# Kernel tuning notes

Measured on AMD Instinct MI355X. Metric: run time of the kernel, lower is better.

## Reference

```python
import jax, jax.numpy as jnp
import numpy as np


def setup_inputs() -> dict:
    key = jax.random.key(0)
    ks = jax.random.split(key, 6)
    B, S, D, F, E = 4, 2048, 1024, 4096, 4
    sd = 1.0 / np.sqrt(D)
    sf = 1.0 / np.sqrt(F)
    return {
        "x": jax.random.normal(ks[0], (B, S, D), jnp.float32),
        "router_w": jax.random.normal(ks[1], (D, E), jnp.float32) * sd,
        "w1": jax.random.normal(ks[2], (E, D, F), jnp.float32) * sd,
        "b1": jnp.zeros((E, F), jnp.float32),
        "w2": jax.random.normal(ks[3], (E, F, D), jnp.float32) * sf,
        "b2": jnp.zeros((E, D), jnp.float32),
    }


def reference(x, router_w, w1, b1, w2, b2):
    # x: [B, S, D] token stream; causal MoE with top-1 routing.
    B, S, D = x.shape
    E = w1.shape[0]
    # Causal routing context: prefix mean over the sequence (causal augmenter).
    denom = jnp.arange(1, S + 1, dtype=x.dtype)[None, :, None]  # [1, S, 1]
    ctx = jnp.cumsum(x, axis=1) / denom                          # [B, S, D]
    logits = jnp.einsum("bsd,de->bse", ctx, router_w)            # [B, S, E]
    probs = jax.nn.softmax(logits, axis=-1)
    idx = jnp.argmax(probs, axis=-1)                             # top-1 expert id [B, S]
    gate = jnp.take_along_axis(probs, idx[..., None], axis=-1)   # [B, S, 1]
    onehot = jax.nn.one_hot(idx, E, dtype=x.dtype)               # [B, S, E]
    # Dispatch/combine: per-expert FFN, masked combine (loop over small fixed E).
    y = jnp.zeros_like(x)
    for e in range(E):
        h = jax.nn.gelu(jnp.einsum("bsd,df->bsf", x, w1[e]) + b1[e])
        y_e = jnp.einsum("bsf,fd->bsd", h, w2[e]) + b2[e]
        y = y + onehot[..., e:e + 1] * y_e
    return gate * y
```

## Files before the change

### kernel.cpp

```cpp
#include <hip/hip_runtime.h>
#include <math.h>

#define B_ 4
#define S_ 2048
#define D_ 1024
#define F_ 4096
#define E_ 4
#define T_ (B_*S_)
#define PCAP_ 9216
#define GCAP_ (PCAP_/16)
#define MB128_ (PCAP_/128)

typedef unsigned short ushort_t;
typedef __attribute__((ext_vector_type(8))) short short8;
typedef __attribute__((ext_vector_type(4))) float f32x4;

__device__ __forceinline__ ushort_t f2bf_rne(float f) {
    unsigned u = __float_as_uint(f);
    unsigned r = 0x7FFFu + ((u >> 16) & 1u);
    u += r;
    return (ushort_t)(u >> 16);
}

__device__ __forceinline__ void gload16(const void* g, void* l) {
    __builtin_amdgcn_global_load_lds(
        (const __attribute__((address_space(1))) unsigned int*)g,
        (__attribute__((address_space(3))) unsigned int*)l, 16, 0, 0);
}


__global__ void k_router(const float* __restrict__ x, const float* __restrict__ rw,
                         float* __restrict__ r, int* __restrict__ counts) {
    if (blockIdx.x == 0 && threadIdx.x < E_) counts[threadIdx.x] = 0;
    int wid = blockIdx.x * 4 + (threadIdx.x >> 6);
    int lane = threadIdx.x & 63;
    const float* xr = x + (size_t)wid * D_;
    float a0 = 0.f, a1 = 0.f, a2 = 0.f, a3 = 0.f;
    for (int i = lane; i < D_; i += 64) {
        float xv = xr[i];
        float4 w = reinterpret_cast<const float4*>(rw)[i];
        a0 += xv * w.x; a1 += xv * w.y; a2 += xv * w.z; a3 += xv * w.w;
    }
    for (int off = 32; off; off >>= 1) {
        a0 += __shfl_down(a0, off, 64);
        a1 += __shfl_down(a1, off, 64);
        a2 += __shfl_down(a2, off, 64);
        a3 += __shfl_down(a3, off, 64);
    }
    if (lane == 0) {
        float4 v; v.x = a0; v.y = a1; v.z = a2; v.w = a3;
        reinterpret_cast<float4*>(r)[wid] = v;
    }
}

__global__ void k_scan(float* __restrict__ r) {
    int b = blockIdx.x >> 2, e = blockIdx.x & 3;
    int lane = threadIdx.x;
    float carry = 0.f;
    for (int c = 0; c < S_ / 64; ++c) {
        int s = c * 64 + lane;
        float* p = r + ((size_t)(b * S_ + s)) * E_ + e;
        float v = *p;
        #pragma unroll
        for (int off = 1; off < 64; off <<= 1) {
            float u = __shfl_up(v, off, 64);
            if (lane >= off) v += u;
        }
        v += carry;
        *p = v;
        carry = __shfl(v, 63, 64);
    }
}

__global__ void k_route(const float* __restrict__ r, float* __restrict__ gate,
                        int* __restrict__ list, int* __restrict__ counts) {
    int t = blockIdx.x * blockDim.x + threadIdx.x;
    if (t >= T_) return;
    int s = t & (S_ - 1);
    float4 l4 = reinterpret_cast<const float4*>(r)[t];
    float inv = 1.f / (float)(s + 1);
    float l[4] = { l4.x * inv, l4.y * inv, l4.z * inv, l4.w * inv };
    int best = 0; float m = l[0];
    #pragma unroll
    for (int e = 1; e < 4; ++e) if (l[e] > m) { m = l[e]; best = e; }
    float sum = 0.f;
    #pragma unroll
    for (int e = 0; e < 4; ++e) sum += expf(l[e] - m);
    gate[t] = 1.f / sum;
    int pos = atomicAdd(&counts[best], 1);
    list[best * T_ + pos] = t;
}

__global__ void k_offs(const int* __restrict__ counts, int* __restrict__ offs,
                       int* __restrict__ pbase) {
    if (threadIdx.x == 0) {
        int a = 0, p = 0;
        pbase[0] = 0;
        for (int e = 0; e < E_; ++e) {
            offs[e] = a; a += counts[e];
            p += (counts[e] + 255) & ~255;
            pbase[e + 1] = p;
        }
    }
}

__global__ __launch_bounds__(256)
void k_gather1(const float* __restrict__ x, const int* __restrict__ list,
               const int* __restrict__ counts, const int* __restrict__ pbase,
               ushort_t* __restrict__ Xb)
{
    constexpr int KB = D_ / 32;
    const int g = blockIdx.x;
    const int r15 = threadIdx.x & 15;
    const int kq = threadIdx.x >> 4;
    const int v = g * 16 + r15;
    int e = 0;
    #pragma unroll
    for (int i = 0; i < E_; ++i) if (v >= pbase[i + 1]) e = i + 1;
    int token = -1;
    if (e < E_) {
        int local = v - pbase[e];
        if (local < counts[e]) token = list[e * T_ + local];
    }
    const float* xr = x + (size_t)(token >= 0 ? token : 0) * D_;
    #pragma unroll
    for (int c8 = 0; c8 < 8; ++c8) {
        const int k = kq * 64 + c8 * 8;
        float vv[8];
        if (token >= 0) {
            float4 u0 = *reinterpret_cast<const float4*>(xr + k);
            float4 u1 = *reinterpret_cast<const float4*>(xr + k + 4);
            vv[0]=u0.x; vv[1]=u0.y; vv[2]=u0.z; vv[3]=u0.w;
            vv[4]=u1.x; vv[5]=u1.y; vv[6]=u1.z; vv[7]=u1.w;
        } else {
            #pragma unroll
            for (int j = 0; j < 8; ++j) vv[j] = 0.f;
        }
        unsigned hw[4];
        #pragma unroll
        for (int j = 0; j < 4; ++j)
            hw[j] = (unsigned)f2bf_rne(vv[2*j]) | ((unsigned)f2bf_rne(vv[2*j+1]) << 16);
        size_t off = (((size_t)g * KB + (k >> 5)) * 64 + ((k >> 3) & 3) * 16 + r15) * 8;
        *reinterpret_cast<uint4*>(Xb + off) = make_uint4(hw[0], hw[1], hw[2], hw[3]);
    }
}

__global__ __launch_bounds__(256)
void k_convert_w1(const float* __restrict__ W, ushort_t* __restrict__ P,
                  int K, int N) {
    const int e = blockIdx.z;
    const int n0 = blockIdx.x * 128;
    const int k0 = blockIdx.y * 32;
    const int kb = blockIdx.y;
    const int NT = N >> 4, KB = K >> 5;
    __shared__ float lf[32 * 128];
    const float* We = W + (size_t)e * K * N;
    const int tid = threadIdx.x;
    #pragma unroll
    for (int i = 0; i < 4; ++i) {
        int q = i * 256 + tid;
        int k = q >> 5, c4 = q & 31;
        float4 v = *reinterpret_cast<const float4*>(We + (size_t)(k0 + k) * N + n0 + c4 * 4);
        *reinterpret_cast<float4*>(lf + k * 128 + c4 * 4) = v;
    }
    __syncthreads();
    #pragma unroll
    for (int p = 0; p < 2; ++p) {
        int q = p * 256 + tid;
        int n = q & 127, kg = q >> 7;
        unsigned hw[4];
        #pragma unroll
        for (int j = 0; j < 8; j += 2) {
            float f0 = lf[(kg * 8 + j) * 128 + n];
            float f1 = lf[(kg * 8 + j + 1) * 128 + n];
            hw[j >> 1] = (unsigned)f2bf_rne(f0) | ((unsigned)f2bf_rne(f1) << 16);
        }
        size_t off = ((((size_t)e * NT + ((n0 + n) >> 4)) * KB + kb) * 64
                      + (kg * 16 + (n & 15))) * 8;
        *reinterpret_cast<uint4*>(P + off) = make_uint4(hw[0], hw[1], hw[2], hw[3]);
    }
}

template<int MODE>
__global__ __launch_bounds__(512)
void k_gI(const ushort_t* __restrict__ A, const ushort_t* __restrict__ Bw,
          const float* __restrict__ bias, float* __restrict__ outF,
          ushort_t* __restrict__ outH,
          const int* __restrict__ list, const int* __restrict__ counts,
          const int* __restrict__ pbase, const float* __restrict__ gate)
{
    constexpr int K    = (MODE == 0) ? D_ : F_;
    constexpr int N    = (MODE == 0) ? F_ : D_;
    constexpr int KSEG = (MODE == 0) ? K : K / 2;
    constexpr int STEPS = KSEG / 32;
    constexpr int KB32 = K / 32;
    constexpr int NT   = N / 16;
    constexpr int KBH  = F_ / 32;

    const int m0g = blockIdx.x * 128;
    if (m0g >= pbase[E_]) return;
    int e = 0;
    #pragma unroll
    for (int i = 1; i <= 3; ++i) if (m0g >= pbase[i]) e = i;
    const int cnt = counts[e];
    const int m0 = m0g - pbase[e];
    if (m0 >= cnt) return;
    const int n0 = blockIdx.y * 128;
    const int kth = (MODE == 0) ? 0 : blockIdx.z;
    const int koff = kth * (KSEG / 32);

    const int tid = threadIdx.x, wid = tid >> 6, lane = tid & 63;
    const int l15 = lane & 15, lkg = lane >> 4;
    const int wr = wid >> 2, wc = wid & 3;
    const int G0 = m0g >> 4;

    __shared__ __align__(16) ushort_t lds[16 * 512];

    const ushort_t* aP = A + ((size_t)(G0 + wid) * KB32 + koff) * 512 + (size_t)lane * 8;
    const ushort_t* bP = Bw + (((size_t)e * NT + (n0 >> 4) + wid) * KB32 + koff) * 512
                            + (size_t)lane * 8;

    f32x4 acc[4][2];
    #pragma unroll
    for (int i = 0; i < 4; ++i)
        #pragma unroll
        for (int j = 0; j < 2; ++j) acc[i][j] = (f32x4){0.f, 0.f, 0.f, 0.f};

    for (int t = 0; t < STEPS; ++t) {
        __syncthreads();
        const size_t so = (size_t)t * 512;
        gload16(aP + so, &lds[wid * 512]);
        gload16(bP + so, &lds[(8 + wid) * 512]);
        __syncthreads();
        short8 av[4], bv[2];
        #pragma unroll
        for (int mi = 0; mi < 4; ++mi)
            av[mi] = *reinterpret_cast<const short8*>(
                &lds[(wr * 4 + mi) * 512 + lane * 8]);
        #pragma unroll
        for (int ni = 0; ni < 2; ++ni)
            bv[ni] = *reinterpret_cast<const short8*>(
                &lds[(8 + wc * 2 + ni) * 512 + lane * 8]);
        #pragma unroll
        for (int mi = 0; mi < 4; ++mi)
            #pragma unroll
            for (int ni = 0; ni < 2; ++ni)
                acc[mi][ni] = __builtin_amdgcn_mfma_f32_16x16x32_bf16(
                    av[mi], bv[ni], acc[mi][ni], 0, 0, 0);
    }

    const float* be = bias + (size_t)e * N;
    if (MODE == 0) {
        #pragma unroll
        for (int mi = 0; mi < 4; ++mi) {
            const int g2 = G0 + wr * 4 + mi;
            #pragma unroll
            for (int rg = 0; rg < 4; ++rg) {
                const int r15o = lkg * 4 + rg;
                #pragma unroll
                for (int ni = 0; ni < 2; ++ni) {
                    const int f = n0 + wc * 32 + ni * 16 + l15;
                    float v = acc[mi][ni][rg] + be[f];
                    float u = 1.5957691216057308f * (v + 0.044715f * v * v * v);
                    v = v / (1.f + __expf(-u));
                    size_t off = (((size_t)g2 * KBH + (f >> 5)) * 64
                                  + ((f >> 3) & 3) * 16 + r15o) * 8 + (f & 7);
                    outH[off] = f2bf_rne(v);
                }
            }
        }
    } else {
        const int* lst = list + (size_t)e * T_;
        #pragma unroll
        for (int mi = 0; mi < 4; ++mi) {
            #pragma unroll
            for (int rg = 0; rg < 4; ++rg) {
                int rm = m0 + wr * 64 + mi * 16 + lkg * 4 + rg;
                if (rm >= cnt) continue;
                int t = lst[rm];
                float gv = gate[t];
                float* crow = outF + (size_t)t * (size_t)N;
                #pragma unroll
                for (int ni = 0; ni < 2; ++ni) {
                    int col = n0 + wc * 32 + ni * 16 + l15;
                    float v = acc[mi][ni][rg] + (kth == 0 ? be[col] : 0.f);
                    atomicAdd(&crow[col], gv * v);
                }
            }
        }
    }
}


extern "C" void kernel_launch(void* const* d_in, const int* in_sizes, int n_in,
                              void* d_out, int out_size, void* d_ws, size_t ws_size,
                              hipStream_t stream) {
    const float* x   = (const float*)d_in[0];
    const float* rw  = (const float*)d_in[1];
    const float* w1  = (const float*)d_in[2];
    const float* b1  = (const float*)d_in[3];
    const float* w2  = (const float*)d_in[4];
    const float* b2  = (const float*)d_in[5];
    float* out = (float*)d_out;

    const size_t HCAP = (size_t)PCAP_ * F_;
    const size_t XCAP = (size_t)PCAP_ * D_;
    const size_t WCAP = (size_t)E_ * D_ * F_;
    const size_t misc = ((size_t)T_ * E_ + T_ + (size_t)E_ * T_) * 4 + 256;
    const size_t need = (HCAP + XCAP + WCAP) * 2 + misc;

    if (ws_size < need) return;

    ushort_t* hB = (ushort_t*)d_ws;
    ushort_t* xB = hB + HCAP;
    ushort_t* wB = xB + XCAP;
    float* r    = (float*)(wB + WCAP);
    float* gate = r + (size_t)T_ * E_;
    int* list   = (int*)(gate + T_);
    int* counts = list + (size_t)E_ * T_;
    int* offs   = counts + E_;
    int* pbase  = offs + E_;

    hipMemsetAsync(out, 0, (size_t)T_ * D_ * 4, stream);

    k_router<<<T_ / 4, 256, 0, stream>>>(x, rw, r, counts);
    k_convert_w1<<<dim3(F_ / 128, D_ / 32, E_), 256, 0, stream>>>(w1, wB, D_, F_);
    k_scan<<<B_ * E_, 64, 0, stream>>>(r);
    k_route<<<T_ / 256, 256, 0, stream>>>(r, gate, list, counts);
    k_offs<<<1, 64, 0, stream>>>(counts, offs, pbase);
    k_gather1<<<GCAP_, 256, 0, stream>>>(x, list, counts, pbase, xB);

    k_gI<0><<<dim3(MB128_, F_ / 128), 512, 0, stream>>>(
        xB, wB, b1, nullptr, hB, list, counts, pbase, nullptr);
    k_convert_w1<<<dim3(D_ / 128, F_ / 32, E_), 256, 0, stream>>>(w2, wB, F_, D_);
    k_gI<1><<<dim3(MB128_, D_ / 128, 2), 512, 0, stream>>>(
        hB, wB, b2, out, nullptr, list, counts, pbase, gate);
}
```

Before: 415.3 us.

## Double-buffer LDS tiles and double K-step in grouped expert GEMM

Rewrites the grouped GEMM main loop to prefetch the next 64-wide K slice into a second LDS buffer while MFMAs consume the current one. The per-iteration sync count drops from two to one, and s_setprio raises wave priority during the MFMA section. This hides global-to-LDS latency, at the cost of quadrupling LDS use to 64KB per block, which may lower occupancy.

```diff
diff --git a/kernel.cpp b/kernel.cpp
--- a/kernel.cpp
+++ b/kernel.cpp
@@ -183,7 +183,7 @@
 
 template<int MODE>
 __global__ __launch_bounds__(512)
-void k_gI(const ushort_t* __restrict__ A, const ushort_t* __restrict__ Bw,
+void k_gJ(const ushort_t* __restrict__ A, const ushort_t* __restrict__ Bw,
           const float* __restrict__ bias, float* __restrict__ outF,
           ushort_t* __restrict__ outH,
           const int* __restrict__ list, const int* __restrict__ counts,
@@ -192,7 +192,7 @@
     constexpr int K    = (MODE == 0) ? D_ : F_;
     constexpr int N    = (MODE == 0) ? F_ : D_;
     constexpr int KSEG = (MODE == 0) ? K : K / 2;
-    constexpr int STEPS = KSEG / 32;
+    constexpr int STEPS = KSEG / 64;
     constexpr int KB32 = K / 32;
     constexpr int NT   = N / 16;
     constexpr int KBH  = F_ / 32;
@@ -214,7 +214,7 @@
     const int wr = wid >> 2, wc = wid & 3;
     const int G0 = m0g >> 4;
 
-    __shared__ __align__(16) ushort_t lds[16 * 512];
+    __shared__ __align__(16) ushort_t lds[2][32 * 512];
 
     const ushort_t* aP = A + ((size_t)(G0 + wid) * KB32 + koff) * 512 + (size_t)lane * 8;
     const ushort_t* bP = Bw + (((size_t)e * NT + (n0 >> 4) + wid) * KB32 + koff) * 512
@@ -226,27 +226,47 @@
         #pragma unroll
         for (int j = 0; j < 2; ++j) acc[i][j] = (f32x4){0.f, 0.f, 0.f, 0.f};
 
+    #pragma unroll
+    for (int kk = 0; kk < 2; ++kk) {
+        gload16(aP + (size_t)kk * 512, &lds[0][(wid * 2 + kk) * 512]);
+        gload16(bP + (size_t)kk * 512, &lds[0][(16 + wid * 2 + kk) * 512]);
+    }
+    __syncthreads();
+
+    int cur = 0;
     for (int t = 0; t < STEPS; ++t) {
+        if (t + 1 < STEPS) {
+            const size_t so = (size_t)(t + 1) * 1024;
+            ushort_t* L = &lds[cur ^ 1][0];
+            #pragma unroll
+            for (int kk = 0; kk < 2; ++kk) {
+                gload16(aP + so + (size_t)kk * 512, L + (wid * 2 + kk) * 512);
+                gload16(bP + so + (size_t)kk * 512, L + (16 + wid * 2 + kk) * 512);
+            }
+        }
+        const ushort_t* L = &lds[cur][0];
+        __builtin_amdgcn_s_setprio(1);
+        #pragma unroll
+        for (int kk = 0; kk < 2; ++kk) {
+            short8 av[4], bv[2];
+            #pragma unroll
+            for (int mi = 0; mi < 4; ++mi)
+                av[mi] = *reinterpret_cast<const short8*>(
+                    &L[((wr * 4 + mi) * 2 + kk) * 512 + lane * 8]);
+            #pragma unroll
+            for (int ni = 0; ni < 2; ++ni)
+                bv[ni] = *reinterpret_cast<const short8*>(
+                    &L[(16 + (wc * 2 + ni) * 2 + kk) * 512 + lane * 8]);
+            #pragma unroll
+            for (int mi = 0; mi < 4; ++mi)
+                #pragma unroll
+                for (int ni = 0; ni < 2; ++ni)
+                    acc[mi][ni] = __builtin_amdgcn_mfma_f32_16x16x32_bf16(
+                        av[mi], bv[ni], acc[mi][ni], 0, 0, 0);
+        }
+        __builtin_amdgcn_s_setprio(0);
         __syncthreads();
-        const size_t so = (size_t)t * 512;
-        gload16(aP + so, &lds[wid * 512]);
-        gload16(bP + so, &lds[(8 + wid) * 512]);
-        __syncthreads();
-        short8 av[4], bv[2];
-        #pragma unroll
-        for (int mi = 0; mi < 4; ++mi)
-            av[mi] = *reinterpret_cast<const short8*>(
-                &lds[(wr * 4 + mi) * 512 + lane * 8]);
-        #pragma unroll
-        for (int ni = 0; ni < 2; ++ni)
-            bv[ni] = *reinterpret_cast<const short8*>(
-                &lds[(8 + wc * 2 + ni) * 512 + lane * 8]);
-        #pragma unroll
-        for (int mi = 0; mi < 4; ++mi)
-            #pragma unroll
-            for (int ni = 0; ni < 2; ++ni)
-                acc[mi][ni] = __builtin_amdgcn_mfma_f32_16x16x32_bf16(
-                    av[mi], bv[ni], acc[mi][ni], 0, 0, 0);
+        cur ^= 1;
     }
 
     const float* be = bias + (size_t)e * N;
@@ -330,9 +350,9 @@
     k_offs<<<1, 64, 0, stream>>>(counts, offs, pbase);
     k_gather1<<<GCAP_, 256, 0, stream>>>(x, list, counts, pbase, xB);
 
-    k_gI<0><<<dim3(MB128_, F_ / 128), 512, 0, stream>>>(
+    k_gJ<0><<<dim3(MB128_, F_ / 128), 512, 0, stream>>>(
         xB, wB, b1, nullptr, hB, list, counts, pbase, nullptr);
     k_convert_w1<<<dim3(D_ / 128, F_ / 32, E_), 256, 0, stream>>>(w2, wB, F_, D_);
-    k_gI<1><<<dim3(MB128_, D_ / 128, 2), 512, 0, stream>>>(
+    k_gJ<1><<<dim3(MB128_, D_ / 128, 2), 512, 0, stream>>>(
         hB, wB, b2, out, nullptr, list, counts, pbase, gate);
 }
```

Measured after the change: 415.3 us. Within noise of the previous version (+0.0%).
